# Performance work log

Measured on AMD Instinct MI355X. Metric: run time of the kernel, lower is better.

Reference implementation:

```python
import jax, jax.numpy as jnp
import numpy as np

B, L, IN_DIM, D, H = 4, 1024, 256, 512, 8
DH = D // H
LARGE_NEG = -10000.0
LN_EPS = 1e-5


def _layernorm(x, g, b):
    mu = jnp.mean(x, axis=-1, keepdims=True)
    var = jnp.mean((x - mu) ** 2, axis=-1, keepdims=True)
    return (x - mu) * jax.lax.rsqrt(var + LN_EPS) * g + b


def setup_inputs() -> dict:
    key = jax.random.key(0)
    ks = jax.random.split(key, 16)
    s = 0.02
    return {
        "x": jax.random.normal(ks[0], (B, L, IN_DIM), jnp.float32),
        "attention_mask": jax.random.bernoulli(ks[1], 0.5, (B, L, L)),
        "adjacency_matrix": jax.random.uniform(ks[2], (B, L, L), jnp.float32),
        "W_fuse": jax.random.normal(ks[3], (D, IN_DIM), jnp.float32) * s,
        "b_fuse": jnp.zeros((D,), jnp.float32),
        "in_proj_w": jax.random.normal(ks[4], (3 * D, D), jnp.float32) * s,
        "in_proj_b": jnp.zeros((3 * D,), jnp.float32),
        "out_w": jax.random.normal(ks[5], (D, D), jnp.float32) * s,
        "out_b": jnp.zeros((D,), jnp.float32),
        "ln1_g": jnp.ones((D,), jnp.float32),
        "ln1_b": jnp.zeros((D,), jnp.float32),
        "ln2_g": jnp.ones((D,), jnp.float32),
        "ln2_b": jnp.zeros((D,), jnp.float32),
        "W1": jax.random.normal(ks[6], (4 * D, D), jnp.float32) * s,
        "b1": jnp.zeros((4 * D,), jnp.float32),
        "W2": jax.random.normal(ks[7], (D, 4 * D), jnp.float32) * s,
        "b2": jnp.zeros((D,), jnp.float32),
        "log_scale": jnp.array(0.0, jnp.float32),  # log(adj_bias_strength=1.0)
    }


def reference(x, attention_mask, adjacency_matrix, W_fuse, b_fuse, in_proj_w,
              in_proj_b, out_w, out_b, ln1_g, ln1_b, ln2_g, ln2_b,
              W1, b1, W2, b2, log_scale):
    # fuse projection (in_dim != d_model)
    x = jnp.einsum("bli,di->bld", x, W_fuse) + b_fuse

    # ensure_self_loops_in_mask: unmask diagonal of fully-masked rows
    eye = jnp.eye(L, dtype=bool)
    row_all = jnp.all(attention_mask, axis=-1)  # [B, L]
    mask = attention_mask & ~(eye[None, :, :] & row_all[:, :, None])

    # additive attention bias: large_neg where masked + scaled clipped adjacency
    bias = jnp.where(mask, LARGE_NEG, 0.0) + \
        jnp.exp(log_scale) * jnp.clip(adjacency_matrix, 0.0, 1.0)  # [B, L, L]

    # --- attention block (pre-norm) ---
    x_norm = _layernorm(x, ln1_g, ln1_b)
    qkv = jnp.einsum("bld,ed->ble", x_norm, in_proj_w) + in_proj_b
    q, k, v = jnp.split(qkv, 3, axis=-1)
    q = q.reshape(B, L, H, DH).transpose(0, 2, 1, 3)  # [B,H,L,DH]
    k = k.reshape(B, L, H, DH).transpose(0, 2, 1, 3)
    v = v.reshape(B, L, H, DH).transpose(0, 2, 1, 3)
    scores = jnp.einsum("bhqd,bhkd->bhqk", q, k) / np.sqrt(DH) + bias[:, None]
    probs = jax.nn.softmax(scores, axis=-1)
    ctx = jnp.einsum("bhqk,bhkd->bhqd", probs, v)
    ctx = ctx.transpose(0, 2, 1, 3).reshape(B, L, D)
    attn_out = jnp.einsum("bld,ed->ble", ctx, out_w) + out_b
    x = x + attn_out

    # --- FFN block (pre-norm) ---
    x_norm = _layernorm(x, ln2_g, ln2_b)
    h = jax.nn.gelu(jnp.einsum("bld,fd->blf", x_norm, W1) + b1, approximate=False)
    ff = jnp.einsum("blf,df->bld", h, W2) + b2
    return x + ff
```

## Files before the change

### kernel.cpp

```cpp
#include <hip/hip_runtime.h>
#include <math.h>

typedef unsigned short UST;
typedef __attribute__((ext_vector_type(8))) short bf16x8;
typedef __attribute__((ext_vector_type(4))) float f32x4;

#define BB 4
#define LL 1024
#define IND 256
#define DD 512
#define HH 8
#define FFD 2048
#define NT (BB*LL)

__device__ __forceinline__ float bf2f(UST u){ return __uint_as_float(((unsigned)u)<<16); }
__device__ __forceinline__ UST f2bf(float f){
  unsigned u = __float_as_uint(f);
  u += 0x7FFFu + ((u>>16)&1u);
  return (UST)(u>>16);
}
__device__ __forceinline__ float ldF(const void* p, long i, int isf32){
  return isf32 ? ((const float*)p)[i] : bf2f(((const UST*)p)[i]);
}
__device__ __forceinline__ bool ldMask(const void* p, long i, int fm){
  if (fm==0) return ((const int*)p)[i] != 0;
  if (fm==1) return ((const unsigned char*)p)[i] != 0;
  if (fm==2) return ((const UST*)p)[i] != 0;
  return ((const float*)p)[i] != 0.f;
}
__device__ __forceinline__ f32x4 mfma16(bf16x8 a, bf16x8 b, f32x4 c){
  return __builtin_amdgcn_mfma_f32_16x16x32_bf16(a, b, c, 0, 0, 0);
}
__device__ __forceinline__ void gld16(const void* g, void* l){
  __builtin_amdgcn_global_load_lds((const __attribute__((address_space(1))) unsigned int*)g,
                                   (__attribute__((address_space(3))) unsigned int*)l, 16, 0, 0);
}

__global__ void detect_k(int* flags, const UST* xh, const unsigned int* mw){
  int lane = threadIdx.x & 63;
  int e0 = (xh[lane] >> 7) & 0xFF;
  int e1 = (xh[64+lane] >> 7) & 0xFF;
  int f32 = __any((e0 >= 140) || (e1 >= 140)) ? 1 : 0;
  unsigned v = mw[lane];
  int w01   = __all(v <= 1u) ? 1 : 0;
  unsigned lo = v & 0xFFFFu, hi = v >> 16;
  int half  = __all((lo==0u||lo==0x3F80u) && (hi==0u||hi==0x3F80u)) ? 1 : 0;
  int wordF = __all(v==0u || v==0x3F800000u) ? 1 : 0;
  int byteB = __all((v & 0xFEFEFEFEu) == 0u) ? 1 : 0;
  if (lane == 0){
    flags[0] = f32;
    flags[1] = w01 ? 0 : (half ? (wordF ? 3 : 2) : (byteB ? 1 : 0));
  }
}

struct CvtArgs { const void* src[11]; UST* dst[11]; int n[11]; };
__global__ __launch_bounds__(256) void cvt_k(const int* flags, CvtArgs a){
  int ti = blockIdx.y;
  int n = a.n[ti];
  long i8 = ((long)blockIdx.x*256 + threadIdx.x)*8;
  if (i8 >= n) return;
  const void* s = a.src[ti]; UST* d = a.dst[ti];
  if (flags[0]){
    const float4* sf = (const float4*)s;
    float4 a0 = sf[i8>>2], a1 = sf[(i8>>2)+1];
    UST o[8] = { f2bf(a0.x),f2bf(a0.y),f2bf(a0.z),f2bf(a0.w),
                 f2bf(a1.x),f2bf(a1.y),f2bf(a1.z),f2bf(a1.w) };
    *(int4*)(d+i8) = *(const int4*)o;
  } else {
    ((int4*)d)[i8>>3] = ((const int4*)s)[i8>>3];
  }
}

__global__ __launch_bounds__(256) void bias_k(const int* flags, const void* mask,
                                              const void* adj, const void* lsp, UST* biasOut){
  int fF = flags[0], fM = flags[1];
  int row = blockIdx.x;
  int i = row & (LL-1);
  long base = (long)row * LL;
  int t = threadIdx.x;
  int j0 = t*4;
  bool mv[4];
  if (fM == 0){
    int4 m4 = *(const int4*)((const int*)mask + base + j0);
    mv[0]=m4.x!=0; mv[1]=m4.y!=0; mv[2]=m4.z!=0; mv[3]=m4.w!=0;
  } else {
    #pragma unroll
    for (int k=0;k<4;++k) mv[k] = ldMask(mask, base + j0 + k, fM);
  }
  float a4[4];
  if (fF){
    float4 av = *(const float4*)((const float*)adj + base + j0);
    a4[0]=av.x; a4[1]=av.y; a4[2]=av.z; a4[3]=av.w;
  } else {
    const UST* ap = (const UST*)adj + base + j0;
    #pragma unroll
    for (int k=0;k<4;++k) a4[k] = bf2f(ap[k]);
  }
  int my = (mv[0]&&mv[1]&&mv[2]&&mv[3]) ? 1 : 0;
  int wa = __all(my);
  __shared__ int sAll[4];
  int w = t >> 6;
  if ((t & 63) == 0) sAll[w] = wa;
  __syncthreads();
  int rowAll = sAll[0] & sAll[1] & sAll[2] & sAll[3];
  float es = expf(ldF(lsp, 0, fF));
  UST o4[4];
  #pragma unroll
  for (int k = 0; k < 4; ++k){
    int j = j0 + k;
    float a = fminf(fmaxf(a4[k], 0.f), 1.f);
    bool eff = mv[k] && !((rowAll != 0) && (j == i));
    o4[k] = f2bf((eff ? -10000.f : 0.f) + es * a);
  }
  *(int2*)(biasOut + base + j0) = *(const int2*)o4;
}

template<int NI, int ACT, int RES, int OUTMODE>
__global__ __launch_bounds__(256) void gemm2_k(const int* flags,
    const UST* __restrict__ A, const UST* __restrict__ Bw, const UST* __restrict__ bias,
    const float* __restrict__ resid, void* Cout, int M, int N, int K){
  constexpr int TN = 32*NI;
  __shared__ UST sA[128*32];
  __shared__ UST sB[TN*32];
  int t = threadIdx.x, w = t>>6, lane = t&63, l15 = lane&15, qd = lane>>4;
  int m0 = blockIdx.x*128, n0 = blockIdx.y*TN;
  int wm = (w&1)*64, wn = (w>>1)*(NI*16);
  f32x4 acc[4][NI];
  #pragma unroll
  for (int mi=0; mi<4; ++mi)
    #pragma unroll
    for (int ni=0; ni<NI; ++ni){ acc[mi][ni][0]=0;acc[mi][ni][1]=0;acc[mi][ni][2]=0;acc[mi][ni][3]=0; }
  int arow = t>>2, acol = (t&3)*8;
  const UST* aSrc = A + (long)(m0+arow)*K + acol;
  const UST* bSrc = Bw + (long)(n0+arow)*K + acol;
  char* ldsA0 = (char*)sA + (w*64)*16;
  char* ldsA1 = (char*)sA + (256 + w*64)*16;
  char* ldsB0 = (char*)sB + (w*64)*16;
  char* ldsB1 = (char*)sB + (256 + w*64)*16;
  for (int k0 = 0; k0 < K; k0 += 32){
    __syncthreads();
    gld16(aSrc + k0, ldsA0);
    gld16(aSrc + 64*K + k0, ldsA1);
    gld16(bSrc + k0, ldsB0);
    if (NI == 4) gld16(bSrc + 64*K + k0, ldsB1);
    __syncthreads();
    bf16x8 afr[4], bfr[NI];
    #pragma unroll
    for (int mi=0; mi<4; ++mi) afr[mi] = *(const bf16x8*)&sA[(wm + mi*16 + l15)*32 + qd*8];
    #pragma unroll
    for (int ni=0; ni<NI; ++ni) bfr[ni] = *(const bf16x8*)&sB[(wn + ni*16 + l15)*32 + qd*8];
    #pragma unroll
    for (int mi=0; mi<4; ++mi)
      #pragma unroll
      for (int ni=0; ni<NI; ++ni)
        acc[mi][ni] = mfma16(afr[mi], bfr[ni], acc[mi][ni]);
  }
  int outF32 = (OUTMODE==1) || (OUTMODE==2 && flags[0]);
  #pragma unroll
  for (int mi=0; mi<4; ++mi){
    #pragma unroll
    for (int ni=0; ni<NI; ++ni){
      int gc = n0 + wn + ni*16 + l15;
      float bv = bf2f(bias[gc]);
      #pragma unroll
      for (int r=0; r<4; ++r){
        int grow = m0 + wm + mi*16 + qd*4 + r;
        float c = acc[mi][ni][r] + bv;
        if (ACT) c = 0.5f*c*(1.f+erff(c*0.70710678118654752f));
        long oi = (long)grow*N + gc;
        if (RES) c += resid[oi];
        if (outF32) ((float*)Cout)[oi] = c;
        else ((UST*)Cout)[oi] = f2bf(c);
      }
    }
  }
}

__global__ __launch_bounds__(256) void ln_k(const int* flags, const float* xin,
    const void* gp, const void* bp, UST* xout){
  int fF = flags[0];
  int row = blockIdx.x, t = threadIdx.x;
  const float* xr = xin + (long)row * DD;
  float v0 = xr[t], v1 = xr[t+256];
  float s = v0+v1, q = v0*v0 + v1*v1;
  #pragma unroll
  for (int off=1; off<64; off<<=1){ s += __shfl_xor(s,off,64); q += __shfl_xor(q,off,64); }
  __shared__ float rs[4], rq[4];
  int w = t>>6;
  if ((t&63)==0){ rs[w]=s; rq[w]=q; }
  __syncthreads();
  float S = rs[0]+rs[1]+rs[2]+rs[3];
  float Q = rq[0]+rq[1]+rq[2]+rq[3];
  float mean = S * (1.f/DD);
  float var  = fmaxf(Q * (1.f/DD) - mean*mean, 0.f);
  float ri = rsqrtf(var + 1e-5f);
  float g0 = ldF(gp, t, fF), b0 = ldF(bp, t, fF);
  float g1 = ldF(gp, t+256, fF), b1 = ldF(bp, t+256, fF);
  xout[(long)row*DD + t]     = f2bf((v0-mean)*ri*g0 + b0);
  xout[(long)row*DD + t+256] = f2bf((v1-mean)*ri*g1 + b1);
}

__global__ __launch_bounds__(256) void repack_v(const UST* __restrict__ qkv, UST* __restrict__ vT){
  int id = blockIdx.x;
  int bh = id & 31, qt = id >> 5;
  int b = bh >> 3, h = bh & 7;
  int t = threadIdx.x, w = t >> 6, lane = t & 63;
  int token = qt*64 + lane;
  const UST* src = qkv + ((long)(b*LL + token))*1536 + 1024 + h*64;
  #pragma unroll
  for (int c = 0; c < 2; ++c){
    int ch = w*2 + c;
    union { int4 v; UST u[8]; } uu;
    uu.v = *(const int4*)(src + ch*8);
    #pragma unroll
    for (int i = 0; i < 8; ++i)
      vT[((long)(bh*64 + ch*8 + i))*LL + token] = uu.u[i];
  }
}

__global__ __launch_bounds__(256) void attn_k(const UST* __restrict__ qkv,
    const UST* __restrict__ vT, const UST* __restrict__ bias, UST* __restrict__ ctx){
  int id = blockIdx.x;
  int b = id & 3, h = (id>>2) & 7, qt = id >> 5;
  int bh = b*HH + h;
  int q0 = qt*64;
  int t = threadIdx.x, w = t>>6, lane = t&63, l15 = lane&15, qd = lane>>4;
  __shared__ UST sK0[64*32], sK1[64*32];
  __shared__ UST sV0[64*32], sV1[64*32];
  __shared__ UST sB0[64*32], sB1[64*32];
  __shared__ UST sP[4][16*72];
  UST* myP = &sP[w][0];

  const UST* qrow = qkv + ((long)(b*LL + q0 + w*16 + l15))*1536 + h*64;
  bf16x8 qf0 = *(const bf16x8*)(qrow + qd*8);
  bf16x8 qf1 = *(const bf16x8*)(qrow + 32 + qd*8);

  int rowS = t>>2, colS = (t&3)*8;
  const UST* kS = qkv + (long)(b*LL + rowS)*1536 + 512 + h*64 + colS;
  const UST* vS = vT + (long)(bh*64 + rowS)*LL + colS;
  const UST* bS = bias + ((long)b<<20) + (long)(q0 + rowS)*LL + colS;
  char* dK0 = (char*)sK0 + w*1024; char* dK1 = (char*)sK1 + w*1024;
  char* dV0 = (char*)sV0 + w*1024; char* dV1 = (char*)sV1 + w*1024;
  char* dB0 = (char*)sB0 + w*1024; char* dB1 = (char*)sB1 + w*1024;

  f32x4 o[4]; float mr_[4], lr_[4];
  #pragma unroll
  for (int i=0;i<4;i++){ o[i][0]=0;o[i][1]=0;o[i][2]=0;o[i][3]=0; mr_[i]=-1e30f; lr_[i]=0.f; }
  const float LOG2E = 1.44269504f;

  for (int kt = 0; kt < 16; ++kt){
    int k0 = kt*64;
    __syncthreads();
    gld16(kS + (long)k0*1536,      dK0);
    gld16(kS + (long)k0*1536 + 32, dK1);
    gld16(vS + k0,                 dV0);
    gld16(vS + k0 + 32,            dV1);
    gld16(bS + k0,                 dB0);
    gld16(bS + k0 + 32,            dB1);
    __syncthreads();

    f32x4 s4[4];
    #pragma unroll
    for (int i=0;i<4;i++){ s4[i][0]=0;s4[i][1]=0;s4[i][2]=0;s4[i][3]=0; }
    #pragma unroll
    for (int ni=0; ni<4; ++ni){
      bf16x8 kf0 = *(const bf16x8*)&sK0[(ni*16+l15)*32 + qd*8];
      bf16x8 kf1 = *(const bf16x8*)&sK1[(ni*16+l15)*32 + qd*8];
      s4[ni] = mfma16(qf0, kf0, s4[ni]);
      s4[ni] = mfma16(qf1, kf1, s4[ni]);
    }
    float sv[4][4];
    #pragma unroll
    for (int ni=0; ni<4; ++ni){
      const UST* sBc = (ni < 2) ? sB0 : sB1;
      int nc = (ni & 1)*16 + l15;
      #pragma unroll
      for (int r=0; r<4; ++r){
        float bzv = bf2f(sBc[(w*16 + qd*4 + r)*32 + nc]);
        sv[ni][r] = fmaf(s4[ni][r], 0.125f, bzv);
      }
    }
    float alpha[4];
    #pragma unroll
    for (int r=0; r<4; ++r){
      float mcur = fmaxf(fmaxf(sv[0][r],sv[1][r]), fmaxf(sv[2][r],sv[3][r]));
      #pragma unroll
      for (int off=1; off<16; off<<=1) mcur = fmaxf(mcur, __shfl_xor(mcur,off,64));
      float mn = fmaxf(mr_[r], mcur);
      alpha[r] = exp2f((mr_[r]-mn)*LOG2E);
      mr_[r] = mn;
      float mn2 = mn*LOG2E;
      float psum = 0.f;
      #pragma unroll
      for (int ni=0; ni<4; ++ni){
        float p = exp2f(fmaf(sv[ni][r], LOG2E, -mn2));
        sv[ni][r] = p; psum += p;
      }
      #pragma unroll
      for (int off=1; off<16; off<<=1) psum += __shfl_xor(psum,off,64);
      lr_[r] = lr_[r]*alpha[r] + psum;
    }
    #pragma unroll
    for (int dn=0; dn<4; ++dn)
      #pragma unroll
      for (int r=0; r<4; ++r) o[dn][r] *= alpha[r];
    #pragma unroll
    for (int ni=0; ni<4; ++ni)
      #pragma unroll
      for (int r=0; r<4; ++r) myP[(qd*4+r)*72 + ni*16 + l15] = f2bf(sv[ni][r]);
    bf16x8 pf0 = *(const bf16x8*)&myP[l15*72 + qd*8];
    bf16x8 pf1 = *(const bf16x8*)&myP[l15*72 + 32 + qd*8];
    #pragma unroll
    for (int dn=0; dn<4; ++dn){
      bf16x8 vf0 = *(const bf16x8*)&sV0[(dn*16+l15)*32 + qd*8];
      bf16x8 vf1 = *(const bf16x8*)&sV1[(dn*16+l15)*32 + qd*8];
      o[dn] = mfma16(pf0, vf0, o[dn]);
      o[dn] = mfma16(pf1, vf1, o[dn]);
    }
  }
  #pragma unroll
  for (int dn=0; dn<4; ++dn){
    #pragma unroll
    for (int r=0; r<4; ++r){
      long oi = ((long)(b*LL + q0 + w*16 + qd*4 + r))*DD + h*64 + dn*16 + l15;
      ctx[oi] = f2bf(o[dn][r] * (1.f/lr_[r]));
    }
  }
}

extern "C" void kernel_launch(void* const* d_in, const int* in_sizes, int n_in,
                              void* d_out, int out_size, void* d_ws, size_t ws_size,
                              hipStream_t stream){
  char* ws = (char*)d_ws;
  size_t o = 0;
  auto alloc = [&](size_t b){ size_t r = o; o += (b + 255) & ~(size_t)255; return r; };
  int*   flags = (int*)(ws + alloc(256));
  size_t biasOff = alloc(8UL<<20);
  size_t qkvOff  = alloc(12UL<<20);
  UST* biasC = (UST*)(ws + biasOff);
  UST* qkv   = (UST*)(ws + qkvOff);
  UST* hb    = (UST*)(ws + biasOff);
  UST* vT    = (UST*)(ws + alloc(4UL<<20));
  UST* xbf   = (UST*)(ws + alloc(2UL<<20));
  UST* wfuse = (UST*)(ws + alloc(131072*2));
  UST* bfuse = (UST*)(ws + alloc(1024));
  UST* ipw   = (UST*)(ws + alloc(786432*2));
  UST* ipb   = (UST*)(ws + alloc(3072*2));
  UST* outw  = (UST*)(ws + alloc(262144*2));
  UST* outb  = (UST*)(ws + alloc(1024));
  UST* w1    = (UST*)(ws + alloc(1048576*2));
  UST* b1    = (UST*)(ws + alloc(4096*2));
  UST* w2    = (UST*)(ws + alloc(1048576*2));
  UST* b2    = (UST*)(ws + alloc(1024));
  float* xf  = (float*)(ws + alloc((size_t)NT*DD*4));
  UST* xn    = (UST*)(ws + alloc((size_t)NT*DD*2));
  UST* ctx   = (UST*)(ws + alloc((size_t)NT*DD*2));
  float* x2  = (float*)(ws + alloc((size_t)NT*DD*4));

  detect_k<<<1, 64, 0, stream>>>(flags, (const UST*)d_in[0], (const unsigned int*)d_in[1]);

  CvtArgs ca;
  const int srcIdx[11] = {0,3,4,5,6,7,8,13,14,15,16};
  UST* dsts[11] = {xbf,wfuse,bfuse,ipw,ipb,outw,outb,w1,b1,w2,b2};
  const int ns[11] = {NT*IND, DD*IND, DD, 3*DD*DD, 3*DD, DD*DD, DD, FFD*DD, FFD, DD*FFD, DD};
  for (int i=0;i<11;i++){ ca.src[i]=d_in[srcIdx[i]]; ca.dst[i]=dsts[i]; ca.n[i]=ns[i]; }
  cvt_k<<<dim3(512,11), 256, 0, stream>>>(flags, ca);

  bias_k<<<BB*LL, 256, 0, stream>>>(flags, d_in[1], d_in[2], d_in[17], biasC);

  gemm2_k<2,0,0,1><<<dim3(32,8), 256, 0, stream>>>(flags, xbf, wfuse, bfuse, nullptr, xf, NT, DD, IND);
  ln_k<<<NT, 256, 0, stream>>>(flags, xf, d_in[9], d_in[10], xn);
  gemm2_k<4,0,0,0><<<dim3(32,12), 256, 0, stream>>>(flags, xn, ipw, ipb, nullptr, qkv, NT, 3*DD, DD);
  repack_v<<<512, 256, 0, stream>>>(qkv, vT);
  attn_k<<<512, 256, 0, stream>>>(qkv, vT, biasC, ctx);
  gemm2_k<2,0,1,1><<<dim3(32,8), 256, 0, stream>>>(flags, ctx, outw, outb, xf, x2, NT, DD, DD);
  ln_k<<<NT, 256, 0, stream>>>(flags, x2, d_in[11], d_in[12], xn);
  gemm2_k<4,1,0,0><<<dim3(32,16), 256, 0, stream>>>(flags, xn, w1, b1, nullptr, hb, NT, FFD, DD);
  gemm2_k<2,0,1,2><<<dim3(32,8), 256, 0, stream>>>(flags, hb, w2, b2, x2, d_out, NT, DD, FFD);
}
```

Baseline: 284.7 us.

## Double-buffer LDS tiles in GEMM and attention kernels to prefetch next tile

Both the GEMM kernel and the flash-attention kernel now keep two LDS buffers for each operand tile. The first tile is loaded before the loop, and each iteration issues the async global-to-LDS load for the next tile right after a single barrier, then computes on the current one. This removes one __syncthreads per iteration and lets the global loads overlap the MFMA and softmax work. The cost is double the LDS footprint: roughly 57KB per block in the attention kernel, which can cut resident blocks per CU. The overlap may also be limited if the compiler inserts conservative vmcnt waits before the LDS reads.

```diff
diff --git a/kernel.cpp b/kernel.cpp
--- a/kernel.cpp
+++ b/kernel.cpp
@@ -120,8 +120,8 @@
     const UST* __restrict__ A, const UST* __restrict__ Bw, const UST* __restrict__ bias,
     const float* __restrict__ resid, void* Cout, int M, int N, int K){
   constexpr int TN = 32*NI;
-  __shared__ UST sA[128*32];
-  __shared__ UST sB[TN*32];
+  __shared__ UST sA[2][128*32];
+  __shared__ UST sB[2][TN*32];
   int t = threadIdx.x, w = t>>6, lane = t&63, l15 = lane&15, qd = lane>>4;
   int m0 = blockIdx.x*128, n0 = blockIdx.y*TN;
   int wm = (w&1)*64, wn = (w>>1)*(NI*16);
@@ -133,22 +133,24 @@
   int arow = t>>2, acol = (t&3)*8;
   const UST* aSrc = A + (long)(m0+arow)*K + acol;
   const UST* bSrc = Bw + (long)(n0+arow)*K + acol;
-  char* ldsA0 = (char*)sA + (w*64)*16;
-  char* ldsA1 = (char*)sA + (256 + w*64)*16;
-  char* ldsB0 = (char*)sB + (w*64)*16;
-  char* ldsB1 = (char*)sB + (256 + w*64)*16;
+  gld16(aSrc,        (char*)sA[0] + w*1024);
+  gld16(aSrc + 64*K, (char*)sA[0] + 4096 + w*1024);
+  gld16(bSrc,        (char*)sB[0] + w*1024);
+  if (NI == 4) gld16(bSrc + 64*K, (char*)sB[0] + 4096 + w*1024);
   for (int k0 = 0; k0 < K; k0 += 32){
+    int cur = (k0>>5)&1, nxt = cur^1;
     __syncthreads();
-    gld16(aSrc + k0, ldsA0);
-    gld16(aSrc + 64*K + k0, ldsA1);
-    gld16(bSrc + k0, ldsB0);
-    if (NI == 4) gld16(bSrc + 64*K + k0, ldsB1);
-    __syncthreads();
+    if (k0 + 32 < K){
+      gld16(aSrc + k0+32,        (char*)sA[nxt] + w*1024);
+      gld16(aSrc + 64*K + k0+32, (char*)sA[nxt] + 4096 + w*1024);
+      gld16(bSrc + k0+32,        (char*)sB[nxt] + w*1024);
+      if (NI == 4) gld16(bSrc + 64*K + k0+32, (char*)sB[nxt] + 4096 + w*1024);
+    }
     bf16x8 afr[4], bfr[NI];
     #pragma unroll
-    for (int mi=0; mi<4; ++mi) afr[mi] = *(const bf16x8*)&sA[(wm + mi*16 + l15)*32 + qd*8];
-    #pragma unroll
-    for (int ni=0; ni<NI; ++ni) bfr[ni] = *(const bf16x8*)&sB[(wn + ni*16 + l15)*32 + qd*8];
+    for (int mi=0; mi<4; ++mi) afr[mi] = *(const bf16x8*)&sA[cur][(wm + mi*16 + l15)*32 + qd*8];
+    #pragma unroll
+    for (int ni=0; ni<NI; ++ni) bfr[ni] = *(const bf16x8*)&sB[cur][(wn + ni*16 + l15)*32 + qd*8];
     #pragma unroll
     for (int mi=0; mi<4; ++mi)
       #pragma unroll
@@ -225,9 +227,9 @@
   int bh = b*HH + h;
   int q0 = qt*64;
   int t = threadIdx.x, w = t>>6, lane = t&63, l15 = lane&15, qd = lane>>4;
-  __shared__ UST sK0[64*32], sK1[64*32];
-  __shared__ UST sV0[64*32], sV1[64*32];
-  __shared__ UST sB0[64*32], sB1[64*32];
+  __shared__ UST sK[2][2][64*32];
+  __shared__ UST sV[2][2][64*32];
+  __shared__ UST sB[2][2][64*32];
   __shared__ UST sP[4][16*72];
   UST* myP = &sP[w][0];
 
@@ -239,40 +241,46 @@
   const UST* kS = qkv + (long)(b*LL + rowS)*1536 + 512 + h*64 + colS;
   const UST* vS = vT + (long)(bh*64 + rowS)*LL + colS;
   const UST* bS = bias + ((long)b<<20) + (long)(q0 + rowS)*LL + colS;
-  char* dK0 = (char*)sK0 + w*1024; char* dK1 = (char*)sK1 + w*1024;
-  char* dV0 = (char*)sV0 + w*1024; char* dV1 = (char*)sV1 + w*1024;
-  char* dB0 = (char*)sB0 + w*1024; char* dB1 = (char*)sB1 + w*1024;
 
   f32x4 o[4]; float mr_[4], lr_[4];
   #pragma unroll
   for (int i=0;i<4;i++){ o[i][0]=0;o[i][1]=0;o[i][2]=0;o[i][3]=0; mr_[i]=-1e30f; lr_[i]=0.f; }
   const float LOG2E = 1.44269504f;
 
+  gld16(kS,      (char*)sK[0][0] + w*1024);
+  gld16(kS + 32, (char*)sK[0][1] + w*1024);
+  gld16(vS,      (char*)sV[0][0] + w*1024);
+  gld16(vS + 32, (char*)sV[0][1] + w*1024);
+  gld16(bS,      (char*)sB[0][0] + w*1024);
+  gld16(bS + 32, (char*)sB[0][1] + w*1024);
+
   for (int kt = 0; kt < 16; ++kt){
+    int cur = kt&1, nxt = cur^1;
     int k0 = kt*64;
     __syncthreads();
-    gld16(kS + (long)k0*1536,      dK0);
-    gld16(kS + (long)k0*1536 + 32, dK1);
-    gld16(vS + k0,                 dV0);
-    gld16(vS + k0 + 32,            dV1);
-    gld16(bS + k0,                 dB0);
-    gld16(bS + k0 + 32,            dB1);
-    __syncthreads();
-
+    if (kt < 15){
+      int kn = k0 + 64;
+      gld16(kS + (long)kn*1536,      (char*)sK[nxt][0] + w*1024);
+      gld16(kS + (long)kn*1536 + 32, (char*)sK[nxt][1] + w*1024);
+      gld16(vS + kn,                 (char*)sV[nxt][0] + w*1024);
+      gld16(vS + kn + 32,            (char*)sV[nxt][1] + w*1024);
+      gld16(bS + kn,                 (char*)sB[nxt][0] + w*1024);
+      gld16(bS + kn + 32,            (char*)sB[nxt][1] + w*1024);
+    }
     f32x4 s4[4];
     #pragma unroll
     for (int i=0;i<4;i++){ s4[i][0]=0;s4[i][1]=0;s4[i][2]=0;s4[i][3]=0; }
     #pragma unroll
     for (int ni=0; ni<4; ++ni){
-      bf16x8 kf0 = *(const bf16x8*)&sK0[(ni*16+l15)*32 + qd*8];
-      bf16x8 kf1 = *(const bf16x8*)&sK1[(ni*16+l15)*32 + qd*8];
+      bf16x8 kf0 = *(const bf16x8*)&sK[cur][0][(ni*16+l15)*32 + qd*8];
+      bf16x8 kf1 = *(const bf16x8*)&sK[cur][1][(ni*16+l15)*32 + qd*8];
       s4[ni] = mfma16(qf0, kf0, s4[ni]);
       s4[ni] = mfma16(qf1, kf1, s4[ni]);
     }
     float sv[4][4];
     #pragma unroll
     for (int ni=0; ni<4; ++ni){
-      const UST* sBc = (ni < 2) ? sB0 : sB1;
+      const UST* sBc = sB[cur][ni>>1];
       int nc = (ni & 1)*16 + l15;
       #pragma unroll
       for (int r=0; r<4; ++r){
@@ -312,8 +320,8 @@
     bf16x8 pf1 = *(const bf16x8*)&myP[l15*72 + 32 + qd*8];
     #pragma unroll
     for (int dn=0; dn<4; ++dn){
-      bf16x8 vf0 = *(const bf16x8*)&sV0[(dn*16+l15)*32 + qd*8];
-      bf16x8 vf1 = *(const bf16x8*)&sV1[(dn*16+l15)*32 + qd*8];
+      bf16x8 vf0 = *(const bf16x8*)&sV[cur][0][(dn*16+l15)*32 + qd*8];
+      bf16x8 vf1 = *(const bf16x8*)&sV[cur][1][(dn*16+l15)*32 + qd*8];
       o[dn] = mfma16(pf0, vf0, o[dn]);
       o[dn] = mfma16(pf1, vf1, o[dn]);
     }
```

After: 274.7 us. 3.5% less time.
